# Performance work log

Measured on AMD Instinct MI355X. Metric: run time of the kernel, lower is better.

## Reference

```python
import jax, jax.numpy as jnp
import numpy as np

TOP_K = 2
NEG_INF = float('-inf')


def setup_inputs() -> dict:
    key = jax.random.key(0)
    kx, kw = jax.random.split(key)
    B, S, D, E = 4, 4096, 2048, 64
    x = jax.random.normal(kx, (B, S, D), dtype=jnp.float32)
    W = jax.random.normal(kw, (E, D), dtype=jnp.float32) * (1.0 / np.sqrt(D))
    b = jnp.zeros((E,), dtype=jnp.float32)
    return {"x": x, "W": W, "b": b}


def reference(x, W, b):
    # logits: [B, S, E] -- small linear gate
    logits = jnp.einsum('bsd,ed->bse', x, W) + b
    B, S, E = logits.shape
    # top-k over experts
    topk_vals, topk_idx = jax.lax.top_k(logits, TOP_K)  # [B,S,K]
    # scatter top-k logits into a -inf filled tensor
    flat_vals = topk_vals.reshape(-1, TOP_K)            # [T, K]
    flat_idx = topk_idx.reshape(-1, TOP_K)              # [T, K]
    T = flat_idx.shape[0]
    sparse = jnp.full((T, E), NEG_INF, dtype=logits.dtype)
    sparse = sparse.at[jnp.arange(T)[:, None], flat_idx].set(flat_vals)
    # softmax over experts; -inf entries become exactly 0
    router_output = jax.nn.softmax(sparse, axis=-1).reshape(B, S, E)
    return router_output, topk_idx
```

## Files before the change

### kernel.cpp

```cpp
#include <hip/hip_runtime.h>
#include <math.h>


#define RD 2048
#define RE 64
#define TB 32
#define NCH 32

typedef __attribute__((ext_vector_type(8))) short bf16x8;
typedef __attribute__((ext_vector_type(4))) float f32x4;
typedef __attribute__((ext_vector_type(4))) unsigned int u32x4;
typedef __attribute__((ext_vector_type(2))) unsigned int u32x2;

__device__ __forceinline__ unsigned short f2b(float f) {
    unsigned int u = __float_as_uint(f);
    unsigned int r = ((u >> 16) & 1u) + 0x7fffu;
    return (unsigned short)((u + r) >> 16);
}
__device__ __forceinline__ float b2f(unsigned short h) {
    return __uint_as_float(((unsigned int)h) << 16);
}

__device__ __forceinline__ int swz(int f) {
    return (f << 2) ^ (((f >> 3) & 7) << 2);
}

__device__ __forceinline__ void cvt8(const f32x4 a, const f32x4 bq,
                                     unsigned int* h, unsigned int* l,
                                     unsigned int* l2) {
    float v[8] = {a.x, a.y, a.z, a.w, bq.x, bq.y, bq.z, bq.w};
#pragma unroll
    for (int j = 0; j < 4; ++j) {
        const float a0 = v[2 * j], a1 = v[2 * j + 1];
        const unsigned short h0 = f2b(a0); const float r0 = a0 - b2f(h0);
        const unsigned short h1 = f2b(a1); const float r1 = a1 - b2f(h1);
        const unsigned short m0 = f2b(r0); const float s0 = r0 - b2f(m0);
        const unsigned short m1 = f2b(r1); const float s1 = r1 - b2f(m1);
        const unsigned short q0 = f2b(s0);
        const unsigned short q1 = f2b(s1);
        h[j]  = (unsigned int)h0 | ((unsigned int)h1 << 16);
        l[j]  = (unsigned int)m0 | ((unsigned int)m1 << 16);
        l2[j] = (unsigned int)q0 | ((unsigned int)q1 << 16);
    }
}

__device__ __forceinline__ void cvt4(const f32x4 a,
                                     unsigned int* h, unsigned int* l,
                                     unsigned int* l2) {
    float v[4] = {a.x, a.y, a.z, a.w};
#pragma unroll
    for (int j = 0; j < 2; ++j) {
        const float a0 = v[2 * j], a1 = v[2 * j + 1];
        const unsigned short h0 = f2b(a0); const float r0 = a0 - b2f(h0);
        const unsigned short h1 = f2b(a1); const float r1 = a1 - b2f(h1);
        const unsigned short m0 = f2b(r0); const float s0 = r0 - b2f(m0);
        const unsigned short m1 = f2b(r1); const float s1 = r1 - b2f(m1);
        const unsigned short q0 = f2b(s0);
        const unsigned short q1 = f2b(s1);
        h[j]  = (unsigned int)h0 | ((unsigned int)h1 << 16);
        l[j]  = (unsigned int)m0 | ((unsigned int)m1 << 16);
        l2[j] = (unsigned int)q0 | ((unsigned int)q1 << 16);
    }
}

__global__ __launch_bounds__(256) void wprep_kernel(
    const float* __restrict__ W, unsigned int* __restrict__ WB)
{
    const int ks = blockIdx.x;
    const int et = threadIdx.x >> 6;
    const int lane = threadIdx.x & 63;
    const int e = et * 16 + (lane & 15);
    const int k0 = ks * 32 + (lane >> 4) * 8;
    const float* src = W + (size_t)e * RD + k0;
    const f32x4 a = *(const f32x4*)(src);
    const f32x4 bq = *(const f32x4*)(src + 4);
    unsigned int h[4], l[4], l2[4];
    cvt8(a, bq, h, l, l2);
    unsigned int* dst = WB + (size_t)((ks * 4 + et) * 3) * 256 + lane * 4;
    *(u32x4*)(dst)       = *(u32x4*)h;
    *(u32x4*)(dst + 256) = *(u32x4*)l;
    *(u32x4*)(dst + 512) = *(u32x4*)l2;
}

__global__ __launch_bounds__(512, 2) void topk_router_kernel(
    const float* __restrict__ x,
    const unsigned int* __restrict__ WB,
    const float* __restrict__ b,
    float* __restrict__ out_router,
    float* __restrict__ out_idx,
    int total_tokens)
{
    const int tid = threadIdx.x;
    const int lane = tid & 63;
    const int wv = __builtin_amdgcn_readfirstlane(tid >> 6);
    const int tt = wv >> 2;
    const int et = wv & 3;
    const int tok0 = blockIdx.x * TB;

    __shared__ __align__(16) unsigned int SM[2][2][2][3][256];

    const int stok = tid >> 4;
    const int part = tid & 15;
    const int tmax = total_tokens - 1;
    const float* gsrc = x + (size_t)min(tok0 + stok, tmax) * RD + part * 4;
    const int s_tt = stok >> 4;
    const int s_ks = part >> 3;
    const int s_f  = ((part >> 1) & 3) * 16 + (stok & 15);
    const int s_off = swz(s_f) + (part & 1) * 2;

    f32x4 acc = {0.f, 0.f, 0.f, 0.f};
    double acc64[4] = {0.0, 0.0, 0.0, 0.0};

    {
        const f32x4 v0 = *(const f32x4*)(gsrc);
        unsigned int h[2], l[2], l2[2];
        cvt4(v0, h, l, l2);
        *(u32x2*)&SM[0][s_tt][s_ks][0][s_off] = *(u32x2*)h;
        *(u32x2*)&SM[0][s_tt][s_ks][1][s_off] = *(u32x2*)l;
        *(u32x2*)&SM[0][s_tt][s_ks][2][s_off] = *(u32x2*)l2;
    }
    f32x4 pf = *(const f32x4*)(gsrc + 64);
    __syncthreads();

#pragma unroll 1
    for (int c = 0; c < NCH; ++c) {
        const int buf = c & 1;
        const int cn = (c + 2 < NCH) ? (c + 2) : 0;
        const f32x4 nx = *(const f32x4*)(gsrc + (size_t)cn * 64);

#pragma unroll
        for (int ks = 0; ks < 2; ++ks) {
            const bf16x8 Ah  = *(const bf16x8*)&SM[buf][tt][ks][0][swz(lane)];
            const bf16x8 Al  = *(const bf16x8*)&SM[buf][tt][ks][1][swz(lane)];
            const bf16x8 Al2 = *(const bf16x8*)&SM[buf][tt][ks][2][swz(lane)];
            const int ksg = c * 2 + ks;
            const unsigned int* wp =
                WB + (size_t)((ksg * 4 + et) * 3) * 256 + lane * 4;
            const bf16x8 Bh  = *(const bf16x8*)(wp);
            const bf16x8 Bl  = *(const bf16x8*)(wp + 256);
            const bf16x8 Bl2 = *(const bf16x8*)(wp + 512);
            acc = __builtin_amdgcn_mfma_f32_16x16x32_bf16(Ah,  Bh,  acc, 0, 0, 0);
            acc = __builtin_amdgcn_mfma_f32_16x16x32_bf16(Ah,  Bl,  acc, 0, 0, 0);
            acc = __builtin_amdgcn_mfma_f32_16x16x32_bf16(Al,  Bh,  acc, 0, 0, 0);
            acc = __builtin_amdgcn_mfma_f32_16x16x32_bf16(Al,  Bl,  acc, 0, 0, 0);
            acc = __builtin_amdgcn_mfma_f32_16x16x32_bf16(Ah,  Bl2, acc, 0, 0, 0);
            acc = __builtin_amdgcn_mfma_f32_16x16x32_bf16(Al2, Bh,  acc, 0, 0, 0);
        }

        if ((c & 7) == 7) {
            acc64[0] += (double)acc.x; acc64[1] += (double)acc.y;
            acc64[2] += (double)acc.z; acc64[3] += (double)acc.w;
            acc = (f32x4){0.f, 0.f, 0.f, 0.f};
        }

        if (c + 1 < NCH) {
            unsigned int h[2], l[2], l2[2];
            cvt4(pf, h, l, l2);
            const int nbuf = (c + 1) & 1;
            *(u32x2*)&SM[nbuf][s_tt][s_ks][0][s_off] = *(u32x2*)h;
            *(u32x2*)&SM[nbuf][s_tt][s_ks][1][s_off] = *(u32x2*)l;
            *(u32x2*)&SM[nbuf][s_tt][s_ks][2][s_off] = *(u32x2*)l2;
        }
        pf = nx;
        __syncthreads();
    }

    double* lg = (double*)&SM[0][0][0][0][0];
#pragma unroll
    for (int r = 0; r < 4; ++r) {
        const int t = tt * 16 + (lane >> 4) * 4 + r;
        const int e = et * 16 + (lane & 15);
        lg[(size_t)t * 66 + e] = acc64[r];
    }
    __syncthreads();

    const double bias = (double)b[lane];

#pragma unroll 1
    for (int i = 0; i < 4; ++i) {
        const int t = wv * 4 + i;
        const int token = tok0 + t;
        const double v = lg[(size_t)t * 66 + lane] + bias;

        double bestv = v;
        int besti = lane;
#pragma unroll
        for (int off = 32; off > 0; off >>= 1) {
            double ov = __shfl_xor(bestv, off, 64);
            int oi = __shfl_xor(besti, off, 64);
            if (ov > bestv || (ov == bestv && oi < besti)) { bestv = ov; besti = oi; }
        }

        double v2 = (lane == besti) ? -INFINITY : v;
        double best2v = v2;
        int best2i = lane;
#pragma unroll
        for (int off = 32; off > 0; off >>= 1) {
            double ov = __shfl_xor(best2v, off, 64);
            int oi = __shfl_xor(best2i, off, 64);
            if (ov > best2v || (ov == best2v && oi < best2i)) { best2v = ov; best2i = oi; }
        }

        const float e2 = expf((float)(best2v - bestv));
        const float denom = 1.0f + e2;
        const float p1v = 1.0f / denom;
        const float p2v = e2 / denom;

        if (token < total_tokens) {
            float outv = 0.0f;
            if (lane == besti) outv = p1v;
            else if (lane == best2i) outv = p2v;
            out_router[(size_t)token * RE + lane] = outv;
            if (lane == 0) {
                out_idx[(size_t)token * 2 + 0] = (float)besti;
                out_idx[(size_t)token * 2 + 1] = (float)best2i;
            }
        }
    }
}

extern "C" void kernel_launch(void* const* d_in, const int* in_sizes, int n_in,
                              void* d_out, int out_size, void* d_ws, size_t ws_size,
                              hipStream_t stream) {
    const float* x = (const float*)d_in[0];
    const float* W = (const float*)d_in[1];
    const float* b = (const float*)d_in[2];

    const int E = in_sizes[2];
    const int D = in_sizes[1] / E;
    const int T = in_sizes[0] / D;
    (void)E; (void)D;

    unsigned int* WB = (unsigned int*)d_ws;
    float* out_router = (float*)d_out;
    float* out_idx = out_router + (size_t)T * RE;

    wprep_kernel<<<64, 256, 0, stream>>>(W, WB);

    const int grid = (T + TB - 1) / TB;
    topk_router_kernel<<<grid, 512, 0, stream>>>(x, WB, b, out_router, out_idx, T);
}
```

Before: 65.60 us.

## Split K across wave groups with smaller token tiles and higher occupancy

Each block now handles 16 tokens instead of 32, and the two wave groups split the 2048-long reduction in half instead of each taking a different token tile. The two partial logit sums are added in shared memory before the top-k step. This doubles the number of blocks and raises the launch-bounds occupancy hint from 2 to 4 blocks per CU, aiming for better latency hiding and load balance. The cost is loading W twice per token relative to the tokens computed, plus an extra reduction step.

```diff
diff --git a/kernel.cpp b/kernel.cpp
--- a/kernel.cpp
+++ b/kernel.cpp
@@ -4,8 +4,8 @@
 
 #define RD 2048
 #define RE 64
-#define TB 32
-#define NCH 32
+#define TB 16
+#define NST 16
 
 typedef __attribute__((ext_vector_type(8))) short bf16x8;
 typedef __attribute__((ext_vector_type(4))) float f32x4;
@@ -82,7 +82,7 @@
     *(u32x4*)(dst + 512) = *(u32x4*)l2;
 }
 
-__global__ __launch_bounds__(512, 2) void topk_router_kernel(
+__global__ __launch_bounds__(512, 4) void topk_router_kernel(
     const float* __restrict__ x,
     const unsigned int* __restrict__ WB,
     const float* __restrict__ b,
@@ -93,19 +93,20 @@
     const int tid = threadIdx.x;
     const int lane = tid & 63;
     const int wv = __builtin_amdgcn_readfirstlane(tid >> 6);
-    const int tt = wv >> 2;
+    const int kh = wv >> 2;
     const int et = wv & 3;
     const int tok0 = blockIdx.x * TB;
 
     __shared__ __align__(16) unsigned int SM[2][2][2][3][256];
 
-    const int stok = tid >> 4;
+    const int s_kh = tid >> 8;
+    const int stok = (tid >> 4) & 15;
     const int part = tid & 15;
     const int tmax = total_tokens - 1;
-    const float* gsrc = x + (size_t)min(tok0 + stok, tmax) * RD + part * 4;
-    const int s_tt = stok >> 4;
+    const float* gsrc = x + (size_t)min(tok0 + stok, tmax) * RD
+                          + s_kh * 1024 + part * 4;
     const int s_ks = part >> 3;
-    const int s_f  = ((part >> 1) & 3) * 16 + (stok & 15);
+    const int s_f  = ((part >> 1) & 3) * 16 + stok;
     const int s_off = swz(s_f) + (part & 1) * 2;
 
     f32x4 acc = {0.f, 0.f, 0.f, 0.f};
@@ -115,25 +116,25 @@
         const f32x4 v0 = *(const f32x4*)(gsrc);
         unsigned int h[2], l[2], l2[2];
         cvt4(v0, h, l, l2);
-        *(u32x2*)&SM[0][s_tt][s_ks][0][s_off] = *(u32x2*)h;
-        *(u32x2*)&SM[0][s_tt][s_ks][1][s_off] = *(u32x2*)l;
-        *(u32x2*)&SM[0][s_tt][s_ks][2][s_off] = *(u32x2*)l2;
+        *(u32x2*)&SM[0][s_kh][s_ks][0][s_off] = *(u32x2*)h;
+        *(u32x2*)&SM[0][s_kh][s_ks][1][s_off] = *(u32x2*)l;
+        *(u32x2*)&SM[0][s_kh][s_ks][2][s_off] = *(u32x2*)l2;
     }
     f32x4 pf = *(const f32x4*)(gsrc + 64);
     __syncthreads();
 
 #pragma unroll 1
-    for (int c = 0; c < NCH; ++c) {
-        const int buf = c & 1;
-        const int cn = (c + 2 < NCH) ? (c + 2) : 0;
+    for (int s = 0; s < NST; ++s) {
+        const int buf = s & 1;
+        const int cn = (s + 2 < NST) ? (s + 2) : 0;
         const f32x4 nx = *(const f32x4*)(gsrc + (size_t)cn * 64);
 
 #pragma unroll
         for (int ks = 0; ks < 2; ++ks) {
-            const bf16x8 Ah  = *(const bf16x8*)&SM[buf][tt][ks][0][swz(lane)];
-            const bf16x8 Al  = *(const bf16x8*)&SM[buf][tt][ks][1][swz(lane)];
-            const bf16x8 Al2 = *(const bf16x8*)&SM[buf][tt][ks][2][swz(lane)];
-            const int ksg = c * 2 + ks;
+            const bf16x8 Ah  = *(const bf16x8*)&SM[buf][kh][ks][0][swz(lane)];
+            const bf16x8 Al  = *(const bf16x8*)&SM[buf][kh][ks][1][swz(lane)];
+            const bf16x8 Al2 = *(const bf16x8*)&SM[buf][kh][ks][2][swz(lane)];
+            const int ksg = kh * 32 + s * 2 + ks;
             const unsigned int* wp =
                 WB + (size_t)((ksg * 4 + et) * 3) * 256 + lane * 4;
             const bf16x8 Bh  = *(const bf16x8*)(wp);
@@ -147,19 +148,19 @@
             acc = __builtin_amdgcn_mfma_f32_16x16x32_bf16(Al2, Bh,  acc, 0, 0, 0);
         }
 
-        if ((c & 7) == 7) {
+        if ((s & 7) == 7) {
             acc64[0] += (double)acc.x; acc64[1] += (double)acc.y;
             acc64[2] += (double)acc.z; acc64[3] += (double)acc.w;
             acc = (f32x4){0.f, 0.f, 0.f, 0.f};
         }
 
-        if (c + 1 < NCH) {
+        if (s + 1 < NST) {
             unsigned int h[2], l[2], l2[2];
             cvt4(pf, h, l, l2);
-            const int nbuf = (c + 1) & 1;
-            *(u32x2*)&SM[nbuf][s_tt][s_ks][0][s_off] = *(u32x2*)h;
-            *(u32x2*)&SM[nbuf][s_tt][s_ks][1][s_off] = *(u32x2*)l;
-            *(u32x2*)&SM[nbuf][s_tt][s_ks][2][s_off] = *(u32x2*)l2;
+            const int nbuf = (s + 1) & 1;
+            *(u32x2*)&SM[nbuf][s_kh][s_ks][0][s_off] = *(u32x2*)h;
+            *(u32x2*)&SM[nbuf][s_kh][s_ks][1][s_off] = *(u32x2*)l;
+            *(u32x2*)&SM[nbuf][s_kh][s_ks][2][s_off] = *(u32x2*)l2;
         }
         pf = nx;
         __syncthreads();
@@ -168,19 +169,20 @@
     double* lg = (double*)&SM[0][0][0][0][0];
 #pragma unroll
     for (int r = 0; r < 4; ++r) {
-        const int t = tt * 16 + (lane >> 4) * 4 + r;
+        const int t = (lane >> 4) * 4 + r;
         const int e = et * 16 + (lane & 15);
-        lg[(size_t)t * 66 + e] = acc64[r];
+        lg[(size_t)(kh * TB + t) * 66 + e] = acc64[r];
     }
     __syncthreads();
 
     const double bias = (double)b[lane];
 
 #pragma unroll 1
-    for (int i = 0; i < 4; ++i) {
-        const int t = wv * 4 + i;
+    for (int i = 0; i < 2; ++i) {
+        const int t = wv * 2 + i;
         const int token = tok0 + t;
-        const double v = lg[(size_t)t * 66 + lane] + bias;
+        const double v = lg[(size_t)t * 66 + lane]
+                       + lg[(size_t)(TB + t) * 66 + lane] + bias;
 
         double bestv = v;
         int besti = lane;
```

Result: faster. 55.19 us (-15.9%).
